# Kernel tuning notes

Hardware: AMD Instinct MI355X
Metric: run time of the kernel (lower is better)

The kernel has to match this reference:

```python
import jax, jax.numpy as jnp
import numpy as np

N = 50000
E_RAND = 800000
IN_DIM, HIDDEN, OUT_DIM, HEADS = 256, 32, 40, 4


def glorot(key, fan_in, fan_out, shape):
    r = np.sqrt(6.0 / (fan_in + fan_out))
    return jax.random.uniform(key, shape, jnp.float32, -r, r)


def setup_inputs() -> dict:
    key = jax.random.key(0)
    ks = jax.random.split(key, 10)
    x = jax.random.normal(ks[0], (N, IN_DIM), jnp.float32)
    # random edges with src != dst, then append self loops (remove+add_self_loops semantics)
    s = jax.random.randint(ks[1], (E_RAND,), 0, N, jnp.int32)
    d = (s + 1 + jax.random.randint(ks[2], (E_RAND,), 0, N - 1, jnp.int32)) % N
    loops = jnp.arange(N, dtype=jnp.int32)
    src = jnp.concatenate([s, loops])
    dst = jnp.concatenate([d, loops])
    lin1 = glorot(ks[3], IN_DIM, HEADS * HIDDEN, (IN_DIM, HEADS * HIDDEN))
    att_q1 = glorot(ks[4], HEADS, HIDDEN, (1, HEADS, HIDDEN))
    att_v1 = glorot(ks[5], HEADS, HIDDEN, (1, HEADS, HIDDEN))
    bias1 = jnp.zeros((HEADS * HIDDEN,), jnp.float32)
    lin2 = glorot(ks[6], HEADS * HIDDEN, HEADS * OUT_DIM, (HEADS * HIDDEN, HEADS * OUT_DIM))
    att_q2 = glorot(ks[7], HEADS, OUT_DIM, (1, HEADS, OUT_DIM))
    att_v2 = glorot(ks[8], HEADS, OUT_DIM, (1, HEADS, OUT_DIM))
    bias2 = jnp.zeros((OUT_DIM,), jnp.float32)
    return {"x": x, "src": src, "dst": dst,
            "lin1": lin1, "att_q1": att_q1, "att_v1": att_v1, "bias1": bias1,
            "lin2": lin2, "att_q2": att_q2, "att_v2": att_v2, "bias2": bias2}


def segment_softmax(e, seg, n):
    # e: [E, H]; softmax grouped by target node seg
    m = jax.ops.segment_max(e, seg, num_segments=n)  # [N, H]
    ex = jnp.exp(e - m[seg])
    s = jax.ops.segment_sum(ex, seg, num_segments=n)
    return ex / (s[seg] + 1e-16)


def ood_gat_conv(x, src, dst, lin, att_q, att_v, bias, concat):
    n = x.shape[0]
    H, C = att_q.shape[1], att_q.shape[2]
    xh = (x @ lin).reshape(n, H, C)                     # [N, H, C]
    alpha = jnp.sum(xh * att_q, axis=-1)                # [N, H]
    sa = jax.nn.sigmoid(alpha)
    w_alpha = 1.0 - jnp.abs(sa[dst] - sa[src])          # [E, H]
    w_beta = jnp.sum(att_v * jax.nn.leaky_relu(xh[dst] + xh[src]), axis=-1)  # [E, H]
    w = segment_softmax(w_alpha * w_beta, dst, n)       # [E, H]
    out = jax.ops.segment_sum(xh[src] * w[..., None], dst, num_segments=n)  # [N, H, C]
    out = out.reshape(n, H * C) if concat else out.mean(axis=1)
    return out + bias


def reference(x, src, dst, lin1, att_q1, att_v1, bias1, lin2, att_q2, att_v2, bias2):
    h = ood_gat_conv(x, src, dst, lin1, att_q1, att_v1, bias1, concat=True)
    h = jax.nn.elu(h)
    out = ood_gat_conv(h, src, dst, lin2, att_q2, att_v2, bias2, concat=False)
    return out
```

## Files before the change

### kernel.cpp

```cpp
#include <hip/hip_runtime.h>
#include <hip/hip_fp16.h>

#define HEADS 4

typedef _Float16 v2h __attribute__((ext_vector_type(2)));

__device__ __forceinline__ float4 ldh4(const __half* p) {
    const uint2 u = *(const uint2*)p;
    const float2 a = __half22float2(*(const __half2*)&u.x);
    const float2 b = __half22float2(*(const __half2*)&u.y);
    return make_float4(a.x, a.y, b.x, b.y);
}

__device__ __forceinline__ __half2 habs2_(__half2 x) {
    unsigned u = *reinterpret_cast<unsigned*>(&x) & 0x7FFF7FFFu;
    return *reinterpret_cast<__half2*>(&u);
}

__device__ __forceinline__ float fdot2_(__half2 a, __half2 b, float c) {
    return __builtin_amdgcn_fdot2(*(v2h*)&a, *(v2h*)&b, c, false);
}

template <int BN, bool AHALF>
__device__ __forceinline__ void gemm_alpha_body(
    const void* __restrict__ Av, const float* __restrict__ B,
    const float* __restrict__ attq, __half* __restrict__ Cout,
    float* __restrict__ sa, int M, int K, int bid) {
    constexpr int BM = 64, BK = 32;
    constexpr int MN = BN / 16;
    constexpr int C = BN / 4;
    __shared__ v2h As2[BK / 2][BM];
    __shared__ v2h Bs2[BK / 2][BN];
    __shared__ float sred[BM][4];
    __shared__ float aq[BN];
    const int m0 = bid * BM;
    const int tid = threadIdx.x;
    const int ty = tid >> 4;
    const int tx = tid & 15;
    for (int i = tid; i < BN; i += 256) aq[i] = attq[i];
    sred[tid >> 2][tid & 3] = 0.f;
    float acc[4][MN] = {};

    for (int kt = 0; kt < K; kt += BK) {
        if (!AHALF) {
            const float* A = (const float*)Av;
            #pragma unroll
            for (int it = 0; it < 2; ++it) {
                const int i = tid + 256 * it;
                const int row = i >> 3;
                const int kc = (i & 7) * 4;
                const int grow = m0 + row;
                float4 v = make_float4(0.f, 0.f, 0.f, 0.f);
                if (grow < M) v = *(const float4*)&A[(size_t)grow * K + kt + kc];
                v2h p0; p0[0] = (_Float16)v.x; p0[1] = (_Float16)v.y;
                v2h p1; p1[0] = (_Float16)v.z; p1[1] = (_Float16)v.w;
                As2[(kc >> 1) + 0][row] = p0;
                As2[(kc >> 1) + 1][row] = p1;
            }
        } else {
            const __half* A = (const __half*)Av;
            #pragma unroll
            for (int it = 0; it < 2; ++it) {
                const int i = tid + 256 * it;
                const int row = i >> 3;
                const int kc = (i & 7) * 4;
                const int grow = m0 + row;
                uint2 u = make_uint2(0u, 0u);
                if (grow < M) u = *(const uint2*)&A[(size_t)grow * K + kt + kc];
                As2[(kc >> 1) + 0][row] = *(v2h*)&u.x;
                As2[(kc >> 1) + 1][row] = *(v2h*)&u.y;
            }
        }
        {
            constexpr int BCH = (BK / 2) * (BN / 4);
            for (int i = tid; i < BCH; i += 256) {
                const int k2 = i / (BN / 4);
                const int n4 = (i % (BN / 4)) * 4;
                const float4 fa = *(const float4*)&B[(size_t)(kt + 2 * k2) * BN + n4];
                const float4 fb = *(const float4*)&B[(size_t)(kt + 2 * k2 + 1) * BN + n4];
                v2h q0; q0[0] = (_Float16)fa.x; q0[1] = (_Float16)fb.x;
                v2h q1; q1[0] = (_Float16)fa.y; q1[1] = (_Float16)fb.y;
                v2h q2; q2[0] = (_Float16)fa.z; q2[1] = (_Float16)fb.z;
                v2h q3; q3[0] = (_Float16)fa.w; q3[1] = (_Float16)fb.w;
                Bs2[k2][n4 + 0] = q0;
                Bs2[k2][n4 + 1] = q1;
                Bs2[k2][n4 + 2] = q2;
                Bs2[k2][n4 + 3] = q3;
            }
        }
        __syncthreads();
        #pragma unroll
        for (int k2 = 0; k2 < BK / 2; ++k2) {
            v2h a_[4], b_[MN];
            #pragma unroll
            for (int i = 0; i < 4; ++i) a_[i] = As2[k2][ty * 4 + i];
            #pragma unroll
            for (int j = 0; j < MN; ++j) b_[j] = Bs2[k2][tx * MN + j];
            #pragma unroll
            for (int i = 0; i < 4; ++i)
                #pragma unroll
                for (int j = 0; j < MN; ++j)
                    acc[i][j] = __builtin_amdgcn_fdot2(a_[i], b_[j], acc[i][j], false);
        }
        __syncthreads();
    }
    const int cbase = tx * MN;
    const int head = cbase / C;
    #pragma unroll
    for (int i = 0; i < 4; ++i) {
        const int grow = m0 + ty * 4 + i;
        if (grow < M) {
            #pragma unroll
            for (int j = 0; j < MN; j += 2) {
                const __half2 h = __floats2half2_rn(acc[i][j], acc[i][j + 1]);
                *(__half2*)&Cout[(size_t)grow * BN + cbase + j] = h;
            }
            float part = 0.f;
            #pragma unroll
            for (int j = 0; j < MN; ++j) part += acc[i][j] * aq[cbase + j];
            atomicAdd(&sred[ty * 4 + i][head], part);
        }
    }
    __syncthreads();
    {
        const int row = m0 + (tid >> 2);
        if (row < M)
            sa[row * 4 + (tid & 3)] =
                1.0f / (1.0f + __expf(-sred[tid >> 2][tid & 3]));
    }
}

__global__ __launch_bounds__(256)
void front_k(const float* __restrict__ x, const float* __restrict__ lin1,
             const float* __restrict__ attq1, __half* __restrict__ xh,
             float* __restrict__ sa, const int* __restrict__ dst,
             int* __restrict__ deg, int M, int K, int MB, int E) {
    if ((int)blockIdx.x < MB) {
        gemm_alpha_body<128, false>(x, lin1, attq1, xh, sa, M, K, blockIdx.x);
    } else {
        const int e = (blockIdx.x - MB) * 256 + threadIdx.x;
        if (e < E) atomicAdd(&deg[dst[e]], 1);
    }
}

__global__ __launch_bounds__(256)
void gemm2_k(const __half* __restrict__ acc16, const float* __restrict__ lin2,
             const float* __restrict__ attq2, __half* __restrict__ xh,
             float* __restrict__ sa, int M, int K) {
    gemm_alpha_body<160, true>(acc16, lin2, attq2, xh, sa, M, K, blockIdx.x);
}

__global__ __launch_bounds__(256)
void scan1_k(const int* __restrict__ deg, int* __restrict__ ro,
             int* __restrict__ bsum, int n) {
    __shared__ int s[256];
    int i = blockIdx.x * 256 + threadIdx.x;
    int v = (i < n) ? deg[i] : 0;
    s[threadIdx.x] = v;
    __syncthreads();
    for (int off = 1; off < 256; off <<= 1) {
        int t = (threadIdx.x >= off) ? s[threadIdx.x - off] : 0;
        __syncthreads();
        s[threadIdx.x] += t;
        __syncthreads();
    }
    if (i < n) ro[i] = s[threadIdx.x] - v;
    if (threadIdx.x == 255) bsum[blockIdx.x] = s[255];
}

__global__ __launch_bounds__(256)
void scan2_k(int* __restrict__ bsum, int nb) {
    __shared__ int s[256];
    int v = (threadIdx.x < nb) ? bsum[threadIdx.x] : 0;
    s[threadIdx.x] = v;
    __syncthreads();
    for (int off = 1; off < 256; off <<= 1) {
        int t = (threadIdx.x >= off) ? s[threadIdx.x - off] : 0;
        __syncthreads();
        s[threadIdx.x] += t;
        __syncthreads();
    }
    if (threadIdx.x < nb) bsum[threadIdx.x] = s[threadIdx.x] - v;
}

__global__ __launch_bounds__(256)
void scan3_k(int* __restrict__ ro, int* __restrict__ cur,
             const int* __restrict__ bsum, int n, int E) {
    int i = blockIdx.x * 256 + threadIdx.x;
    if (i < n) {
        int r = ro[i] + bsum[i >> 8];
        ro[i] = r;
        cur[i] = r;
    }
    if (i == 0) ro[n] = E;
}

__global__ __launch_bounds__(256)
void scatter_idx_k(const int* __restrict__ src, const int* __restrict__ dst,
                   int* __restrict__ cur, int* __restrict__ csr_src, int E) {
    int e = blockIdx.x * 256 + threadIdx.x;
    if (e >= E) return;
    int d = dst[e];
    int pos = atomicAdd(&cur[d], 1);
    csr_src[pos] = src[e];
}

template <int C, bool CONCAT>
__global__ __launch_bounds__(256)
void fused_edge_k(const int* __restrict__ ro, const int* __restrict__ csr_src,
                  const __half* __restrict__ xh, const float* __restrict__ sa,
                  const float* __restrict__ attv, const float* __restrict__ bias,
                  void* __restrict__ outp, int n) {
    constexpr int HC = 4 * C;
    constexpr int QH = C / 4;
    constexpr int CHUNK = 64;
    constexpr bool DUAL = (C <= 32);
    const int wid = threadIdx.x >> 6;
    const int lane = threadIdx.x & 63;
    const int node = blockIdx.x * 4 + wid;

    __shared__ float wbuf[4][CHUNK * 4];
    __shared__ int sibuf[4][CHUNK];
    __shared__ __half2 avs[HC / 2];
    for (int i = threadIdx.x; i < HC / 2; i += 256)
        avs[i] = __floats2half2_rn(attv[2 * i], attv[2 * i + 1]);
    __syncthreads();
    if (node >= n) return;

    const int s0 = ro[node], s1 = ro[node + 1];

    const int e_loc = lane >> 2;
    const int h_l = lane & 3;
    const float sad = sa[node * 4 + h_l];
    const __half2 c505 = __floats2half2_rn(0.505f, 0.505f);
    const __half2 c495 = __floats2half2_rn(0.495f, 0.495f);

    __half2 xd[QH * 2];
    {
        const __half* p = &xh[(size_t)node * HC + h_l * C];
        #pragma unroll
        for (int i = 0; i < QH; ++i) {
            const uint2 u = *(const uint2*)&p[i * 4];
            xd[2 * i] = *(const __half2*)&u.x;
            xd[2 * i + 1] = *(const __half2*)&u.y;
        }
    }

    const int half_ = DUAL ? (lane >> 5) : 0;
    const int q = DUAL ? (lane & 31) : lane;
    const int h_a = (q < C) ? (q / QH) : 0;

    float4 acc = make_float4(0.f, 0.f, 0.f, 0.f);
    float ssum = 0.f;

    for (int base = s0; base < s1; base += CHUNK) {
        const int cnt = min(CHUNK, s1 - base);
        const int npass = (cnt + 15) >> 4;
        for (int p = 0; p < npass; ++p) {
            const int eidx = p * 16 + e_loc;
            const int j = base + eidx;
            float w = 0.f;
            int si = 0;
            if (j < s1) {
                si = csr_src[j];
                const float sas = sa[si * 4 + h_l];
                const float wa = 1.0f - fabsf(sad - sas);
                const __half* xs = &xh[(size_t)si * HC + h_l * C];
                float wb = 0.f;
                #pragma unroll
                for (int i = 0; i < QH; ++i) {
                    const uint2 u = *(const uint2*)&xs[i * 4];
                    const __half2 a0 = *(const __half2*)&u.x;
                    const __half2 a1 = *(const __half2*)&u.y;
                    const __half2 t0 = __hadd2(a0, xd[2 * i]);
                    const __half2 t1 = __hadd2(a1, xd[2 * i + 1]);
                    const __half2 l0 = __hfma2(t0, c505, __hmul2(habs2_(t0), c495));
                    const __half2 l1 = __hfma2(t1, c505, __hmul2(habs2_(t1), c495));
                    wb = fdot2_(l0, avs[h_l * QH * 2 + 2 * i], wb);
                    wb = fdot2_(l1, avs[h_l * QH * 2 + 2 * i + 1], wb);
                }
                w = __expf(fminf(wa * wb, 60.f));
                ssum += w;
            }
            wbuf[wid][eidx * 4 + h_l] = w;
            if (h_l == 0) sibuf[wid][eidx] = si;
        }
        const int padded = npass << 4;
        if (q < C) {
            if (DUAL) {
                for (int i = 0; i < padded; i += 8) {
                    const int e0 = i + half_, e1 = i + half_ + 2;
                    const int e2 = i + half_ + 4, e3 = i + half_ + 6;
                    const int i0 = sibuf[wid][e0], i1 = sibuf[wid][e1];
                    const int i2 = sibuf[wid][e2], i3 = sibuf[wid][e3];
                    const float w0 = wbuf[wid][e0 * 4 + h_a];
                    const float w1 = wbuf[wid][e1 * 4 + h_a];
                    const float w2 = wbuf[wid][e2 * 4 + h_a];
                    const float w3 = wbuf[wid][e3 * 4 + h_a];
                    const float4 v0 = ldh4(&xh[(size_t)i0 * HC + q * 4]);
                    const float4 v1 = ldh4(&xh[(size_t)i1 * HC + q * 4]);
                    const float4 v2 = ldh4(&xh[(size_t)i2 * HC + q * 4]);
                    const float4 v3 = ldh4(&xh[(size_t)i3 * HC + q * 4]);
                    acc.x += w0 * v0.x + w1 * v1.x + w2 * v2.x + w3 * v3.x;
                    acc.y += w0 * v0.y + w1 * v1.y + w2 * v2.y + w3 * v3.y;
                    acc.z += w0 * v0.z + w1 * v1.z + w2 * v2.z + w3 * v3.z;
                    acc.w += w0 * v0.w + w1 * v1.w + w2 * v2.w + w3 * v3.w;
                }
            } else {
                for (int i = 0; i < padded; i += 4) {
                    const int i0 = sibuf[wid][i],     i1 = sibuf[wid][i + 1];
                    const int i2 = sibuf[wid][i + 2], i3 = sibuf[wid][i + 3];
                    const float w0 = wbuf[wid][(i + 0) * 4 + h_a];
                    const float w1 = wbuf[wid][(i + 1) * 4 + h_a];
                    const float w2 = wbuf[wid][(i + 2) * 4 + h_a];
                    const float w3 = wbuf[wid][(i + 3) * 4 + h_a];
                    const float4 v0 = ldh4(&xh[(size_t)i0 * HC + q * 4]);
                    const float4 v1 = ldh4(&xh[(size_t)i1 * HC + q * 4]);
                    const float4 v2 = ldh4(&xh[(size_t)i2 * HC + q * 4]);
                    const float4 v3 = ldh4(&xh[(size_t)i3 * HC + q * 4]);
                    acc.x += w0 * v0.x + w1 * v1.x + w2 * v2.x + w3 * v3.x;
                    acc.y += w0 * v0.y + w1 * v1.y + w2 * v2.y + w3 * v3.y;
                    acc.z += w0 * v0.z + w1 * v1.z + w2 * v2.z + w3 * v3.z;
                    acc.w += w0 * v0.w + w1 * v1.w + w2 * v2.w + w3 * v3.w;
                }
            }
        }
    }

    if (DUAL) {
        acc.x += __shfl_xor(acc.x, 32, 64);
        acc.y += __shfl_xor(acc.y, 32, 64);
        acc.z += __shfl_xor(acc.z, 32, 64);
        acc.w += __shfl_xor(acc.w, 32, 64);
    }

    #pragma unroll
    for (int off = 4; off < 64; off <<= 1) ssum += __shfl_xor(ssum, off, 64);
    const float stot = __shfl(ssum, h_a, 64);
    const float inv = 1.0f / (stot + 1e-20f);
    acc.x *= inv; acc.y *= inv; acc.z *= inv; acc.w *= inv;

    if (CONCAT) {
        if (q < C && half_ == 0) {
            const float4 b = ((const float4*)bias)[q];
            float4 v = make_float4(acc.x + b.x, acc.y + b.y, acc.z + b.z, acc.w + b.w);
            v.x = v.x > 0.f ? v.x : __expf(v.x) - 1.0f;
            v.y = v.y > 0.f ? v.y : __expf(v.y) - 1.0f;
            v.z = v.z > 0.f ? v.z : __expf(v.z) - 1.0f;
            v.w = v.w > 0.f ? v.w : __expf(v.w) - 1.0f;
            __half* o16 = (__half*)outp;
            const __half2 h01 = __floats2half2_rn(v.x, v.y);
            const __half2 h23 = __floats2half2_rn(v.z, v.w);
            uint2 u;
            u.x = *(const unsigned*)&h01;
            u.y = *(const unsigned*)&h23;
            *(uint2*)&o16[(size_t)node * HC + q * 4] = u;
        }
    } else {
        const int qq = (q < QH) ? q : 0;
        const float x1 = __shfl(acc.x, qq + QH, 64);
        const float y1 = __shfl(acc.y, qq + QH, 64);
        const float z1 = __shfl(acc.z, qq + QH, 64);
        const float w1 = __shfl(acc.w, qq + QH, 64);
        const float x2 = __shfl(acc.x, qq + 2 * QH, 64);
        const float y2 = __shfl(acc.y, qq + 2 * QH, 64);
        const float z2 = __shfl(acc.z, qq + 2 * QH, 64);
        const float w2 = __shfl(acc.w, qq + 2 * QH, 64);
        const float x3 = __shfl(acc.x, qq + 3 * QH, 64);
        const float y3 = __shfl(acc.y, qq + 3 * QH, 64);
        const float z3 = __shfl(acc.z, qq + 3 * QH, 64);
        const float w3 = __shfl(acc.w, qq + 3 * QH, 64);
        if (q < QH && half_ == 0) {
            float* of = (float*)outp;
            const float4 b = ((const float4*)bias)[q];
            float4 v;
            v.x = 0.25f * (acc.x + x1 + x2 + x3) + b.x;
            v.y = 0.25f * (acc.y + y1 + y2 + y3) + b.y;
            v.z = 0.25f * (acc.z + z1 + z2 + z3) + b.z;
            v.w = 0.25f * (acc.w + w1 + w2 + w3) + b.w;
            *(float4*)&of[(size_t)node * C + q * 4] = v;
        }
    }
}

extern "C" void kernel_launch(void* const* d_in, const int* in_sizes, int n_in,
                              void* d_out, int out_size, void* d_ws, size_t ws_size,
                              hipStream_t stream) {
    const float* x      = (const float*)d_in[0];
    const int*   src    = (const int*)d_in[1];
    const int*   dst    = (const int*)d_in[2];
    const float* lin1   = (const float*)d_in[3];
    const float* att_q1 = (const float*)d_in[4];
    const float* att_v1 = (const float*)d_in[5];
    const float* bias1  = (const float*)d_in[6];
    const float* lin2   = (const float*)d_in[7];
    const float* att_q2 = (const float*)d_in[8];
    const float* att_v2 = (const float*)d_in[9];
    const float* bias2  = (const float*)d_in[10];
    float* outp = (float*)d_out;

    const int n = in_sizes[0] / 256;
    const int E = in_sizes[1];
    const int nh = n * HEADS;
    const int NB = (n + 255) / 256;

    char* wsb = (char*)d_ws;
    size_t o = 0;
    __half* xh    = (__half*)(wsb + o); o += (size_t)n * 160 * 2;
    __half* acc16 = (__half*)(wsb + o); o += (size_t)n * 128 * 2;
    float* sa     = (float*)(wsb + o); o += (size_t)nh * 4;
    int* csr_src  = (int*)(wsb + o); o += (size_t)E * 4;
    int* deg      = (int*)(wsb + o); o += (size_t)n * 4;
    int* ro       = (int*)(wsb + o); o += (size_t)(n + 1) * 4;
    int* cur      = (int*)(wsb + o); o += (size_t)n * 4;
    int* bsum     = (int*)(wsb + o); o += 256 * 4;

    dim3 blk(256);
    const int EG = (E + 255) / 256;
    const int MB = (n + 63) / 64;

    hipMemsetAsync(deg, 0, (size_t)n * 4, stream);
    front_k<<<MB + EG, blk, 0, stream>>>(x, lin1, att_q1, xh, sa, dst, deg,
                                         n, 256, MB, E);
    scan1_k<<<NB, blk, 0, stream>>>(deg, ro, bsum, n);
    scan2_k<<<1, blk, 0, stream>>>(bsum, NB);
    scan3_k<<<NB, blk, 0, stream>>>(ro, cur, bsum, n, E);
    scatter_idx_k<<<EG, blk, 0, stream>>>(src, dst, cur, csr_src, E);

    fused_edge_k<32, true><<<(n + 3) / 4, blk, 0, stream>>>(ro, csr_src, xh, sa, att_v1, bias1, acc16, n);

    gemm2_k<<<MB, blk, 0, stream>>>(acc16, lin2, att_q2, xh, sa, n, 128);
    fused_edge_k<40, false><<<(n + 3) / 4, blk, 0, stream>>>(ro, csr_src, xh, sa, att_v2, bias2, outp, n);
}
```

Before: 331.9 us.

## Pre-convert weights to half2, merge scan passes, fuse GEMM1 with CSR scatter

Result: faster. 320.2 us (-3.5%).

```diff
diff --git a/kernel.cpp b/kernel.cpp
--- a/kernel.cpp
+++ b/kernel.cpp
@@ -23,7 +23,7 @@
 
 template <int BN, bool AHALF>
 __device__ __forceinline__ void gemm_alpha_body(
-    const void* __restrict__ Av, const float* __restrict__ B,
+    const void* __restrict__ Av, const __half2* __restrict__ Bh,
     const float* __restrict__ attq, __half* __restrict__ Cout,
     float* __restrict__ sa, int M, int K, int bid) {
     constexpr int BM = 64, BK = 32;
@@ -76,16 +76,8 @@
             for (int i = tid; i < BCH; i += 256) {
                 const int k2 = i / (BN / 4);
                 const int n4 = (i % (BN / 4)) * 4;
-                const float4 fa = *(const float4*)&B[(size_t)(kt + 2 * k2) * BN + n4];
-                const float4 fb = *(const float4*)&B[(size_t)(kt + 2 * k2 + 1) * BN + n4];
-                v2h q0; q0[0] = (_Float16)fa.x; q0[1] = (_Float16)fb.x;
-                v2h q1; q1[0] = (_Float16)fa.y; q1[1] = (_Float16)fb.y;
-                v2h q2; q2[0] = (_Float16)fa.z; q2[1] = (_Float16)fb.z;
-                v2h q3; q3[0] = (_Float16)fa.w; q3[1] = (_Float16)fb.w;
-                Bs2[k2][n4 + 0] = q0;
-                Bs2[k2][n4 + 1] = q1;
-                Bs2[k2][n4 + 2] = q2;
-                Bs2[k2][n4 + 3] = q3;
+                *(float4*)&Bs2[k2][n4] =
+                    *(const float4*)&Bh[(size_t)(kt / 2 + k2) * BN + n4];
             }
         }
         __syncthreads();
@@ -131,23 +123,28 @@
 }
 
 __global__ __launch_bounds__(256)
-void front_k(const float* __restrict__ x, const float* __restrict__ lin1,
-             const float* __restrict__ attq1, __half* __restrict__ xh,
-             float* __restrict__ sa, const int* __restrict__ dst,
-             int* __restrict__ deg, int M, int K, int MB, int E) {
-    if ((int)blockIdx.x < MB) {
-        gemm_alpha_body<128, false>(x, lin1, attq1, xh, sa, M, K, blockIdx.x);
+void prep_k(const float* __restrict__ lin1, const float* __restrict__ lin2,
+            __half2* __restrict__ l1h, __half2* __restrict__ l2h,
+            const int* __restrict__ dst, int* __restrict__ deg,
+            int CVB, int E) {
+    if ((int)blockIdx.x < CVB) {
+        const int t = blockIdx.x * 256 + threadIdx.x;
+        if (t < 128 * 128) {
+            const int k2 = t >> 7, nn = t & 127;
+            l1h[t] = __floats2half2_rn(lin1[(2 * k2) * 128 + nn],
+                                       lin1[(2 * k2 + 1) * 128 + nn]);
+        } else {
+            const int u = t - 128 * 128;
+            if (u < 64 * 160) {
+                const int k2 = u / 160, nn = u % 160;
+                l2h[u] = __floats2half2_rn(lin2[(2 * k2) * 160 + nn],
+                                           lin2[(2 * k2 + 1) * 160 + nn]);
+            }
+        }
     } else {
-        const int e = (blockIdx.x - MB) * 256 + threadIdx.x;
+        const int e = ((int)blockIdx.x - CVB) * 256 + threadIdx.x;
         if (e < E) atomicAdd(&deg[dst[e]], 1);
     }
-}
-
-__global__ __launch_bounds__(256)
-void gemm2_k(const __half* __restrict__ acc16, const float* __restrict__ lin2,
-             const float* __restrict__ attq2, __half* __restrict__ xh,
-             float* __restrict__ sa, int M, int K) {
-    gemm_alpha_body<160, true>(acc16, lin2, attq2, xh, sa, M, K, blockIdx.x);
 }
 
 __global__ __launch_bounds__(256)
@@ -169,9 +166,10 @@
 }
 
 __global__ __launch_bounds__(256)
-void scan2_k(int* __restrict__ bsum, int nb) {
+void scan23_k(int* __restrict__ ro, int* __restrict__ cur,
+              const int* __restrict__ bsum, int n, int E, int nb) {
     __shared__ int s[256];
-    int v = (threadIdx.x < nb) ? bsum[threadIdx.x] : 0;
+    int v = ((int)threadIdx.x < nb) ? bsum[threadIdx.x] : 0;
     s[threadIdx.x] = v;
     __syncthreads();
     for (int off = 1; off < 256; off <<= 1) {
@@ -180,15 +178,10 @@
         s[threadIdx.x] += t;
         __syncthreads();
     }
-    if (threadIdx.x < nb) bsum[threadIdx.x] = s[threadIdx.x] - v;
-}
-
-__global__ __launch_bounds__(256)
-void scan3_k(int* __restrict__ ro, int* __restrict__ cur,
-             const int* __restrict__ bsum, int n, int E) {
-    int i = blockIdx.x * 256 + threadIdx.x;
+    const int pref = (blockIdx.x == 0) ? 0 : s[blockIdx.x - 1];
+    const int i = blockIdx.x * 256 + threadIdx.x;
     if (i < n) {
-        int r = ro[i] + bsum[i >> 8];
+        const int r = ro[i] + pref;
         ro[i] = r;
         cur[i] = r;
     }
@@ -196,13 +189,28 @@
 }
 
 __global__ __launch_bounds__(256)
-void scatter_idx_k(const int* __restrict__ src, const int* __restrict__ dst,
-                   int* __restrict__ cur, int* __restrict__ csr_src, int E) {
-    int e = blockIdx.x * 256 + threadIdx.x;
-    if (e >= E) return;
-    int d = dst[e];
-    int pos = atomicAdd(&cur[d], 1);
-    csr_src[pos] = src[e];
+void front2_k(const float* __restrict__ x, const __half2* __restrict__ l1h,
+              const float* __restrict__ attq1, __half* __restrict__ xh,
+              float* __restrict__ sa, const int* __restrict__ src,
+              const int* __restrict__ dst, int* __restrict__ cur,
+              int* __restrict__ csr_src, int M, int K, int MB, int E) {
+    if ((int)blockIdx.x < MB) {
+        gemm_alpha_body<128, false>(x, l1h, attq1, xh, sa, M, K, blockIdx.x);
+    } else {
+        const int e = ((int)blockIdx.x - MB) * 256 + threadIdx.x;
+        if (e < E) {
+            const int d = dst[e];
+            const int pos = atomicAdd(&cur[d], 1);
+            csr_src[pos] = src[e];
+        }
+    }
+}
+
+__global__ __launch_bounds__(256)
+void gemm2_k(const __half* __restrict__ acc16, const __half2* __restrict__ l2h,
+             const float* __restrict__ attq2, __half* __restrict__ xh,
+             float* __restrict__ sa, int M, int K) {
+    gemm_alpha_body<160, true>(acc16, l2h, attq2, xh, sa, M, K, blockIdx.x);
 }
 
 template <int C, bool CONCAT>
@@ -406,29 +414,29 @@
 
     char* wsb = (char*)d_ws;
     size_t o = 0;
-    __half* xh    = (__half*)(wsb + o); o += (size_t)n * 160 * 2;
-    __half* acc16 = (__half*)(wsb + o); o += (size_t)n * 128 * 2;
-    float* sa     = (float*)(wsb + o); o += (size_t)nh * 4;
-    int* csr_src  = (int*)(wsb + o); o += (size_t)E * 4;
-    int* deg      = (int*)(wsb + o); o += (size_t)n * 4;
-    int* ro       = (int*)(wsb + o); o += (size_t)(n + 1) * 4;
-    int* cur      = (int*)(wsb + o); o += (size_t)n * 4;
-    int* bsum     = (int*)(wsb + o); o += 256 * 4;
+    __half* xh     = (__half*)(wsb + o); o += (size_t)n * 160 * 2;
+    __half* acc16  = (__half*)(wsb + o); o += (size_t)n * 128 * 2;
+    float* sa      = (float*)(wsb + o); o += (size_t)nh * 4;
+    int* csr_src   = (int*)(wsb + o); o += (size_t)E * 4;
+    int* deg       = (int*)(wsb + o); o += (size_t)n * 4;
+    int* ro        = (int*)(wsb + o); o += (size_t)(n + 1) * 4;
+    int* cur       = (int*)(wsb + o); o += (size_t)n * 4;
+    int* bsum      = (int*)(wsb + o); o += 256 * 4;
+    __half2* l1h   = (__half2*)(wsb + o); o += (size_t)128 * 128 * 4;
+    __half2* l2h   = (__half2*)(wsb + o); o += (size_t)64 * 160 * 4;
 
     dim3 blk(256);
     const int EG = (E + 255) / 256;
     const int MB = (n + 63) / 64;
+    const int CVB = (128 * 128 + 64 * 160 + 255) / 256;
 
     hipMemsetAsync(deg, 0, (size_t)n * 4, stream);
-    front_k<<<MB + EG, blk, 0, stream>>>(x, lin1, att_q1, xh, sa, dst, deg,
-                                         n, 256, MB, E);
+    prep_k<<<CVB + EG, blk, 0, stream>>>(lin1, lin2, l1h, l2h, dst, deg, CVB, E);
     scan1_k<<<NB, blk, 0, stream>>>(deg, ro, bsum, n);
-    scan2_k<<<1, blk, 0, stream>>>(bsum, NB);
-    scan3_k<<<NB, blk, 0, stream>>>(ro, cur, bsum, n, E);
-    scatter_idx_k<<<EG, blk, 0, stream>>>(src, dst, cur, csr_src, E);
-
+    scan23_k<<<NB, blk, 0, stream>>>(ro, cur, bsum, n, E, NB);
+    front2_k<<<MB + EG, blk, 0, stream>>>(x, l1h, att_q1, xh, sa, src, dst,
+                                          cur, csr_src, n, 256, MB, E);
     fused_edge_k<32, true><<<(n + 3) / 4, blk, 0, stream>>>(ro, csr_src, xh, sa, att_v1, bias1, acc16, n);
-
-    gemm2_k<<<MB, blk, 0, stream>>>(acc16, lin2, att_q2, xh, sa, n, 128);
+    gemm2_k<<<MB, blk, 0, stream>>>(acc16, l2h, att_q2, xh, sa, n, 128);
     fused_edge_k<40, false><<<(n + 3) / 4, blk, 0, stream>>>(ro, csr_src, xh, sa, att_v2, bias2, outp, n);
 }
```
